# Optimization experiments

Measured on AMD Instinct MI355X. Metric: run time of the kernel, lower is better.

The kernel has to match this reference:

```python
import jax, jax.numpy as jnp
import numpy as np

ALPHA = 0.2          # LeakyReLU negative slope
NEG_INF = -9e15      # mask value from the torch source
N, F_IN, F_OUT = 8192, 128, 64


def setup_inputs() -> dict:
    key = jax.random.key(0)
    k1, k2, k3, k4, k5 = jax.random.split(key, 5)
    X = jax.random.normal(k1, (N, F_IN), dtype=jnp.float32)
    A = jax.random.randint(k2, (N, N), 0, 2, dtype=jnp.int32)  # 0/1 adjacency
    W = jax.random.normal(k3, (F_IN, F_OUT), dtype=jnp.float32) * 0.05
    a1 = jax.random.normal(k4, (F_OUT,), dtype=jnp.float32) * 0.05
    a2 = jax.random.normal(k5, (F_OUT,), dtype=jnp.float32) * 0.05
    return {"X": X, "A": A, "W": W, "a1": a1, "a2": a2}


def reference(X, A, W, a1, a2):
    # h = W(X)  (Linear, no bias)
    h = X @ W                                   # (N, F_out)
    # a([h_i || h_j]) == h_i @ a1 + h_j @ a2  (split of the 2F attention vector)
    s1 = h @ a1                                 # (N,)
    s2 = h @ a2                                 # (N,)
    e = jax.nn.leaky_relu(s1[:, None] + s2[None, :], ALPHA)  # (N, N)
    att = jnp.where(A > 0, e, NEG_INF)
    att = jax.nn.softmax(att, axis=1)           # row-wise masked softmax
    # dropout p=0.0 -> identity
    return att @ h                              # (N, F_out)
```

## Files before the change

### kernel.cpp

```cpp
#include <hip/hip_runtime.h>
#include <hip/hip_bf16.h>

#define NV 8192
#define FIN 128
#define FOUT 64

typedef __attribute__((ext_vector_type(8))) short short8;
typedef __attribute__((ext_vector_type(4))) float floatx4;

__device__ __forceinline__ uint f2bf_u(float f) {
  uint u = __float_as_uint(f);
  return (u + 0x7FFFu + ((u >> 16) & 1u)) >> 16;
}
__device__ __forceinline__ float bf2f(ushort b) {
  return __uint_as_float(((uint)b) << 16);
}

__global__ void k0_detect(const uint* __restrict__ X, int* __restrict__ flag) {
  const int lane = threadIdx.x & 63;
  uint u = X[lane];
  uint e = (u >> 7) & 0xFF;
  bool ok = (e >= 100u) && (e <= 135u);
  unsigned long long b = __ballot(ok);
  if (lane == 0) *flag = (__builtin_popcountll(b) >= 48) ? 1 : 0;
}

__global__ __launch_bounds__(256) void k1_proj(
    const void* __restrict__ Xv, const void* __restrict__ Wv,
    const void* __restrict__ a1v_, const void* __restrict__ a2v_,
    ushort* __restrict__ HtT, float* __restrict__ s1, float* __restrict__ s2,
    const int* __restrict__ flagp)
{
  const int is_bf16 = *flagp;
  const int wave = threadIdx.x >> 6;
  const int lane = threadIdx.x & 63;
  const int i0 = blockIdx.x * 64 + wave * 16;
  const int col = lane & 15;
  const int q   = lane >> 4;

  short8 bfrag[4][4];
  float a1f[4], a2f[4];
  if (is_bf16) {
    const ushort* W = (const ushort*)Wv;
#pragma unroll
    for (int nt = 0; nt < 4; ++nt)
#pragma unroll
      for (int kc = 0; kc < 4; ++kc) {
        short8 b;
#pragma unroll
        for (int j = 0; j < 8; ++j)
          b[j] = (short)W[(kc*32 + q*8 + j)*FOUT + nt*16 + col];
        bfrag[nt][kc] = b;
      }
#pragma unroll
    for (int nt = 0; nt < 4; ++nt) {
      a1f[nt] = bf2f(((const ushort*)a1v_)[nt*16 + col]);
      a2f[nt] = bf2f(((const ushort*)a2v_)[nt*16 + col]);
    }
  } else {
    const float* W = (const float*)Wv;
#pragma unroll
    for (int nt = 0; nt < 4; ++nt)
#pragma unroll
      for (int kc = 0; kc < 4; ++kc) {
        short8 b;
#pragma unroll
        for (int j = 0; j < 8; ++j)
          b[j] = (short)f2bf_u(W[(kc*32 + q*8 + j)*FOUT + nt*16 + col]);
        bfrag[nt][kc] = b;
      }
#pragma unroll
    for (int nt = 0; nt < 4; ++nt) {
      a1f[nt] = ((const float*)a1v_)[nt*16 + col];
      a2f[nt] = ((const float*)a2v_)[nt*16 + col];
    }
  }

  floatx4 acc[4] = {{0.f,0.f,0.f,0.f},{0.f,0.f,0.f,0.f},
                    {0.f,0.f,0.f,0.f},{0.f,0.f,0.f,0.f}};
#pragma unroll
  for (int kc = 0; kc < 4; ++kc) {
    short8 a;
    if (is_bf16) {
      a = *(const short8*)&((const ushort*)Xv)[(size_t)(i0 + col)*FIN + kc*32 + q*8];
    } else {
      const float* X = (const float*)Xv;
      float4 x0 = *(const float4*)&X[(size_t)(i0 + col)*FIN + kc*32 + q*8];
      float4 x1 = *(const float4*)&X[(size_t)(i0 + col)*FIN + kc*32 + q*8 + 4];
      a[0] = (short)f2bf_u(x0.x); a[1] = (short)f2bf_u(x0.y);
      a[2] = (short)f2bf_u(x0.z); a[3] = (short)f2bf_u(x0.w);
      a[4] = (short)f2bf_u(x1.x); a[5] = (short)f2bf_u(x1.y);
      a[6] = (short)f2bf_u(x1.z); a[7] = (short)f2bf_u(x1.w);
    }
#pragma unroll
    for (int nt = 0; nt < 4; ++nt)
      acc[nt] = __builtin_amdgcn_mfma_f32_16x16x32_bf16(a, bfrag[nt][kc], acc[nt], 0, 0, 0);
  }

  float s1p[4] = {0,0,0,0}, s2p[4] = {0,0,0,0};
#pragma unroll
  for (int nt = 0; nt < 4; ++nt) {
    ushort4 pk;
    pk.x = (ushort)f2bf_u(acc[nt][0]);
    pk.y = (ushort)f2bf_u(acc[nt][1]);
    pk.z = (ushort)f2bf_u(acc[nt][2]);
    pk.w = (ushort)f2bf_u(acc[nt][3]);
    *(ushort4*)&HtT[(size_t)(nt*16 + col)*NV + i0 + q*4] = pk;
#pragma unroll
    for (int reg = 0; reg < 4; ++reg) {
      s1p[reg] += acc[nt][reg] * a1f[nt];
      s2p[reg] += acc[nt][reg] * a2f[nt];
    }
  }
#pragma unroll
  for (int m = 1; m < 16; m <<= 1)
#pragma unroll
    for (int reg = 0; reg < 4; ++reg) {
      s1p[reg] += __shfl_xor(s1p[reg], m, 64);
      s2p[reg] += __shfl_xor(s2p[reg], m, 64);
    }
  if (col == 0)
#pragma unroll
    for (int reg = 0; reg < 4; ++reg) {
      s1[i0 + q*4 + reg] = s1p[reg];
      s2[i0 + q*4 + reg] = s2p[reg];
    }
}

#define CT 256
#define NTILES (NV / CT)
#define PSTR (CT + 8)

__global__ __launch_bounds__(256) void k2_attn(
    const int* __restrict__ A, const ushort* __restrict__ HtT,
    const float* __restrict__ s1g, const float* __restrict__ s2g,
    void* __restrict__ outv, const int* __restrict__ flagp)
{
  __shared__ __align__(16) ushort Pl[16 * PSTR];
  __shared__ __align__(16) ushort Hl[64 * PSTR];
  __shared__ float Lrow[16];

  const int is_bf16 = *flagp;
  const int tid   = threadIdx.x;
  const int wave  = tid >> 6;
  const int lane  = tid & 63;
  const int i0    = blockIdx.x * 16;
  const int rbase = wave * 4;
  const int q     = lane >> 4;
  const int mcol  = lane & 15;
  const int srow  = tid >> 5;
  const int scol  = (tid & 31) * 8;

  float s1v[4];
#pragma unroll
  for (int rr = 0; rr < 4; ++rr) s1v[rr] = s1g[i0 + rbase + rr];

  float Lp[4] = {0,0,0,0};
  floatx4 acc = {0.f,0.f,0.f,0.f};

  for (int t = 0; t < NTILES; ++t) {
    const int c0 = t * CT;
    int4 av[4];
#pragma unroll
    for (int rr = 0; rr < 4; ++rr)
      av[rr] = *(const int4*)&A[(size_t)(i0 + rbase + rr)*NV + c0 + lane*4];
    float4 s2v = *(const float4*)&s2g[c0 + lane*4];
    short8 hv[8];
#pragma unroll
    for (int it = 0; it < 8; ++it)
      hv[it] = *(const short8*)&HtT[(size_t)(srow + 8*it)*NV + c0 + scol];

    __syncthreads();

#pragma unroll
    for (int rr = 0; rr < 4; ++rr) {
      const int4 a = av[rr];
      const float s1r = s1v[rr];
      float x0 = s1r + s2v.x, x1 = s1r + s2v.y, x2 = s1r + s2v.z, x3 = s1r + s2v.w;
      float w0 = a.x ? __expf(fmaxf(x0, 0.2f*x0)) : 0.f;
      float w1 = a.y ? __expf(fmaxf(x1, 0.2f*x1)) : 0.f;
      float w2 = a.z ? __expf(fmaxf(x2, 0.2f*x2)) : 0.f;
      float w3 = a.w ? __expf(fmaxf(x3, 0.2f*x3)) : 0.f;
      Lp[rr] += (w0 + w1) + (w2 + w3);
      uint2 pk;
      pk.x = f2bf_u(w0) | (f2bf_u(w1) << 16);
      pk.y = f2bf_u(w2) | (f2bf_u(w3) << 16);
      *(uint2*)&Pl[(rbase + rr)*PSTR + lane*4] = pk;
    }
#pragma unroll
    for (int it = 0; it < 8; ++it)
      *(short8*)&Hl[(srow + 8*it)*PSTR + scol] = hv[it];

    __syncthreads();

#pragma unroll
    for (int kc = 0; kc < 8; ++kc) {
      short8 af = *(const short8*)&Pl[mcol*PSTR + kc*32 + q*8];
      short8 bf = *(const short8*)&Hl[(wave*16 + mcol)*PSTR + kc*32 + q*8];
      acc = __builtin_amdgcn_mfma_f32_16x16x32_bf16(af, bf, acc, 0, 0, 0);
    }
  }

#pragma unroll
  for (int m = 1; m < 64; m <<= 1)
#pragma unroll
    for (int rr = 0; rr < 4; ++rr) Lp[rr] += __shfl_xor(Lp[rr], m, 64);
  if (lane == 0)
#pragma unroll
    for (int rr = 0; rr < 4; ++rr) Lrow[rbase + rr] = Lp[rr];
  __syncthreads();

#pragma unroll
  for (int reg = 0; reg < 4; ++reg) {
    int r = q*4 + reg;
    float v = acc[reg] / Lrow[r];
    if (is_bf16)
      ((ushort*)outv)[(size_t)(i0 + r)*FOUT + wave*16 + mcol] = (ushort)f2bf_u(v);
    else
      ((float*)outv)[(size_t)(i0 + r)*FOUT + wave*16 + mcol] = v;
  }
}

extern "C" void kernel_launch(void* const* d_in, const int* in_sizes, int n_in,
                              void* d_out, int out_size, void* d_ws, size_t ws_size,
                              hipStream_t stream) {
  const void* X  = d_in[0];
  const int*  A  = (const int*)d_in[1];
  const void* W  = d_in[2];
  const void* a1 = d_in[3];
  const void* a2 = d_in[4];

  char* ws = (char*)d_ws;
  ushort* HtT  = (ushort*)ws;
  float*  s1   = (float*)(ws + (size_t)FOUT*NV*2);
  float*  s2   = s1 + NV;
  int*    flag = (int*)(s2 + NV);

  hipLaunchKernelGGL(k0_detect, dim3(1), dim3(64), 0, stream,
                     (const uint*)X, flag);
  hipLaunchKernelGGL(k1_proj, dim3(NV/64), dim3(256), 0, stream,
                     X, W, a1, a2, HtT, s1, s2, flag);
  hipLaunchKernelGGL(k2_attn, dim3(NV/16), dim3(256), 0, stream,
                     A, HtT, s1, s2, d_out, flag);
}
```

Baseline: 383.8 us.

## Split attention column tiles across waves and drop per-tile block barriers

Each wave now takes its own 64-column slice of every 256-column tile and computes all 16 rows by 64 features of partial output. It reads the H fragments straight from global memory instead of staging them in shared memory, and it keeps a private P buffer, so both per-tile __syncthreads are gone. The four per-wave partial accumulators and row sums are combined through shared memory once at the end. The price is more accumulator registers and uncoalesced strided global loads of HtT done by every wave.

```diff
diff --git a/kernel.cpp b/kernel.cpp
--- a/kernel.cpp
+++ b/kernel.cpp
@@ -129,48 +129,51 @@
 
 #define CT 256
 #define NTILES (NV / CT)
-#define PSTR (CT + 8)
+#define PST 72
 
 __global__ __launch_bounds__(256) void k2_attn(
     const int* __restrict__ A, const ushort* __restrict__ HtT,
     const float* __restrict__ s1g, const float* __restrict__ s2g,
     void* __restrict__ outv, const int* __restrict__ flagp)
 {
-  __shared__ __align__(16) ushort Pl[16 * PSTR];
-  __shared__ __align__(16) ushort Hl[64 * PSTR];
-  __shared__ float Lrow[16];
+  __shared__ __align__(16) ushort Pl[4][16 * PST];
+  __shared__ __align__(16) float Red[4][16][64];
+  __shared__ float Lw[4][16];
 
   const int is_bf16 = *flagp;
-  const int tid   = threadIdx.x;
-  const int wave  = tid >> 6;
-  const int lane  = tid & 63;
-  const int i0    = blockIdx.x * 16;
-  const int rbase = wave * 4;
-  const int q     = lane >> 4;
-  const int mcol  = lane & 15;
-  const int srow  = tid >> 5;
-  const int scol  = (tid & 31) * 8;
+  const int tid  = threadIdx.x;
+  const int wave = tid >> 6;
+  const int lane = tid & 63;
+  const int i0   = blockIdx.x * 16;
+  const int q    = lane >> 4;
+  const int mcol = lane & 15;
+
+  ushort* Pw = &Pl[wave][0];
 
   float s1v[4];
 #pragma unroll
-  for (int rr = 0; rr < 4; ++rr) s1v[rr] = s1g[i0 + rbase + rr];
+  for (int rr = 0; rr < 4; ++rr) s1v[rr] = s1g[i0 + q*4 + rr];
+
+  size_t arow[4], hrow[4];
+#pragma unroll
+  for (int rr = 0; rr < 4; ++rr)
+    arow[rr] = (size_t)(i0 + q*4 + rr) * NV + mcol*4;
+#pragma unroll
+  for (int nt = 0; nt < 4; ++nt)
+    hrow[nt] = (size_t)(nt*16 + mcol) * NV + q*8;
 
   float Lp[4] = {0,0,0,0};
-  floatx4 acc = {0.f,0.f,0.f,0.f};
-
+  floatx4 acc[4] = {{0.f,0.f,0.f,0.f},{0.f,0.f,0.f,0.f},
+                    {0.f,0.f,0.f,0.f},{0.f,0.f,0.f,0.f}};
+
+#pragma unroll 2
   for (int t = 0; t < NTILES; ++t) {
-    const int c0 = t * CT;
+    const int c = t*CT + wave*64;
     int4 av[4];
 #pragma unroll
     for (int rr = 0; rr < 4; ++rr)
-      av[rr] = *(const int4*)&A[(size_t)(i0 + rbase + rr)*NV + c0 + lane*4];
-    float4 s2v = *(const float4*)&s2g[c0 + lane*4];
-    short8 hv[8];
-#pragma unroll
-    for (int it = 0; it < 8; ++it)
-      hv[it] = *(const short8*)&HtT[(size_t)(srow + 8*it)*NV + c0 + scol];
-
-    __syncthreads();
+      av[rr] = *(const int4*)&A[arow[rr] + c];
+    float4 s2v = *(const float4*)&s2g[c + mcol*4];
 
 #pragma unroll
     for (int rr = 0; rr < 4; ++rr) {
@@ -185,39 +188,57 @@
       uint2 pk;
       pk.x = f2bf_u(w0) | (f2bf_u(w1) << 16);
       pk.y = f2bf_u(w2) | (f2bf_u(w3) << 16);
-      *(uint2*)&Pl[(rbase + rr)*PSTR + lane*4] = pk;
-    }
-#pragma unroll
-    for (int it = 0; it < 8; ++it)
-      *(short8*)&Hl[(srow + 8*it)*PSTR + scol] = hv[it];
-
-    __syncthreads();
-
-#pragma unroll
-    for (int kc = 0; kc < 8; ++kc) {
-      short8 af = *(const short8*)&Pl[mcol*PSTR + kc*32 + q*8];
-      short8 bf = *(const short8*)&Hl[(wave*16 + mcol)*PSTR + kc*32 + q*8];
-      acc = __builtin_amdgcn_mfma_f32_16x16x32_bf16(af, bf, acc, 0, 0, 0);
-    }
-  }
-
-#pragma unroll
-  for (int m = 1; m < 64; m <<= 1)
+      *(uint2*)&Pw[(q*4 + rr)*PST + mcol*4] = pk;
+    }
+
+#pragma unroll
+    for (int kc2 = 0; kc2 < 2; ++kc2) {
+      short8 af = *(const short8*)&Pw[mcol*PST + kc2*32 + q*8];
+#pragma unroll
+      for (int nt = 0; nt < 4; ++nt) {
+        short8 bf = *(const short8*)&HtT[hrow[nt] + c + kc2*32];
+        acc[nt] = __builtin_amdgcn_mfma_f32_16x16x32_bf16(af, bf, acc[nt], 0, 0, 0);
+      }
+    }
+  }
+
+#pragma unroll
+  for (int m = 1; m < 16; m <<= 1)
 #pragma unroll
     for (int rr = 0; rr < 4; ++rr) Lp[rr] += __shfl_xor(Lp[rr], m, 64);
-  if (lane == 0)
-#pragma unroll
-    for (int rr = 0; rr < 4; ++rr) Lrow[rbase + rr] = Lp[rr];
+  if (mcol == 0)
+#pragma unroll
+    for (int rr = 0; rr < 4; ++rr) Lw[wave][q*4 + rr] = Lp[rr];
+
+#pragma unroll
+  for (int nt = 0; nt < 4; ++nt)
+#pragma unroll
+    for (int reg = 0; reg < 4; ++reg)
+      Red[wave][q*4 + reg][nt*16 + mcol] = acc[nt][reg];
+
   __syncthreads();
 
-#pragma unroll
-  for (int reg = 0; reg < 4; ++reg) {
-    int r = q*4 + reg;
-    float v = acc[reg] / Lrow[r];
-    if (is_bf16)
-      ((ushort*)outv)[(size_t)(i0 + r)*FOUT + wave*16 + mcol] = (ushort)f2bf_u(v);
-    else
-      ((float*)outv)[(size_t)(i0 + r)*FOUT + wave*16 + mcol] = v;
+  {
+    const int r  = tid >> 4;
+    const int fb = (tid & 15) * 4;
+    float4 s = {0.f, 0.f, 0.f, 0.f};
+    float L = 0.f;
+#pragma unroll
+    for (int w = 0; w < 4; ++w) {
+      float4 v = *(const float4*)&Red[w][r][fb];
+      s.x += v.x; s.y += v.y; s.z += v.z; s.w += v.w;
+      L += Lw[w][r];
+    }
+    const float inv = __frcp_rn(L);
+    s.x *= inv; s.y *= inv; s.z *= inv; s.w *= inv;
+    if (is_bf16) {
+      ushort4 pk;
+      pk.x = (ushort)f2bf_u(s.x); pk.y = (ushort)f2bf_u(s.y);
+      pk.z = (ushort)f2bf_u(s.z); pk.w = (ushort)f2bf_u(s.w);
+      *(ushort4*)&((ushort*)outv)[(size_t)(i0 + r)*FOUT + fb] = pk;
+    } else {
+      *(float4*)&((float*)outv)[(size_t)(i0 + r)*FOUT + fb] = s;
+    }
   }
 }
 
```

After: 404.5 us. +5.4%, slower.

## Prefetch next attention tile into registers and shrink column tile to 128

Applied to the files above, without the earlier changes.

The attention kernel now loads the next tile's adjacency, s2 and H values into registers right after the LDS barrier, so those global loads overlap the MFMA work on the current tile. The column tile drops from 256 to 128 and thread mapping changes to one row per 16 threads with 8 columns each, which halves LDS use. Launch bounds now request 6 blocks per multiprocessor. The aim is to hide the latency of streaming the adjacency matrix from memory, at the cost of twice as many loop iterations and barriers.

```diff
diff --git a/kernel.cpp b/kernel.cpp
--- a/kernel.cpp
+++ b/kernel.cpp
@@ -127,97 +127,104 @@
     }
 }
 
-#define CT 256
-#define NTILES (NV / CT)
-#define PSTR (CT + 8)
-
-__global__ __launch_bounds__(256) void k2_attn(
+#define CT 128
+#define NT (NV / CT)
+#define PST 136
+
+__global__ __launch_bounds__(256, 6) void k2_attn(
     const int* __restrict__ A, const ushort* __restrict__ HtT,
     const float* __restrict__ s1g, const float* __restrict__ s2g,
     void* __restrict__ outv, const int* __restrict__ flagp)
 {
-  __shared__ __align__(16) ushort Pl[16 * PSTR];
-  __shared__ __align__(16) ushort Hl[64 * PSTR];
+  __shared__ __align__(16) ushort Pl[16 * PST];
+  __shared__ __align__(16) ushort Hl[64 * PST];
   __shared__ float Lrow[16];
 
   const int is_bf16 = *flagp;
-  const int tid   = threadIdx.x;
-  const int wave  = tid >> 6;
-  const int lane  = tid & 63;
-  const int i0    = blockIdx.x * 16;
-  const int rbase = wave * 4;
-  const int q     = lane >> 4;
-  const int mcol  = lane & 15;
-  const int srow  = tid >> 5;
-  const int scol  = (tid & 31) * 8;
-
-  float s1v[4];
-#pragma unroll
-  for (int rr = 0; rr < 4; ++rr) s1v[rr] = s1g[i0 + rbase + rr];
-
-  float Lp[4] = {0,0,0,0};
-  floatx4 acc = {0.f,0.f,0.f,0.f};
-
-  for (int t = 0; t < NTILES; ++t) {
-    const int c0 = t * CT;
-    int4 av[4];
-#pragma unroll
-    for (int rr = 0; rr < 4; ++rr)
-      av[rr] = *(const int4*)&A[(size_t)(i0 + rbase + rr)*NV + c0 + lane*4];
-    float4 s2v = *(const float4*)&s2g[c0 + lane*4];
-    short8 hv[8];
-#pragma unroll
-    for (int it = 0; it < 8; ++it)
-      hv[it] = *(const short8*)&HtT[(size_t)(srow + 8*it)*NV + c0 + scol];
-
+  const int tid  = threadIdx.x;
+  const int wave = tid >> 6;
+  const int lane = tid & 63;
+  const int i0   = blockIdx.x * 16;
+  const int q    = lane >> 4;
+  const int mcol = lane & 15;
+  const int r    = tid >> 4;
+  const int cb   = (tid & 15) * 8;
+
+  const float s1r = s1g[i0 + r];
+  const size_t abase = (size_t)(i0 + r) * NV + cb;
+
+  float Lp = 0.f;
+  floatx4 acc = {0.f, 0.f, 0.f, 0.f};
+
+  int4 av0 = *(const int4*)&A[abase];
+  int4 av1 = *(const int4*)&A[abase + 4];
+  float4 sv0 = *(const float4*)&s2g[cb];
+  float4 sv1 = *(const float4*)&s2g[cb + 4];
+  short8 hv[4];
+#pragma unroll
+  for (int it = 0; it < 4; ++it)
+    hv[it] = *(const short8*)&HtT[(size_t)(r + 16*it) * NV + cb];
+
+  for (int t = 0; t < NT; ++t) {
     __syncthreads();
 
-#pragma unroll
-    for (int rr = 0; rr < 4; ++rr) {
-      const int4 a = av[rr];
-      const float s1r = s1v[rr];
-      float x0 = s1r + s2v.x, x1 = s1r + s2v.y, x2 = s1r + s2v.z, x3 = s1r + s2v.w;
-      float w0 = a.x ? __expf(fmaxf(x0, 0.2f*x0)) : 0.f;
-      float w1 = a.y ? __expf(fmaxf(x1, 0.2f*x1)) : 0.f;
-      float w2 = a.z ? __expf(fmaxf(x2, 0.2f*x2)) : 0.f;
-      float w3 = a.w ? __expf(fmaxf(x3, 0.2f*x3)) : 0.f;
-      Lp[rr] += (w0 + w1) + (w2 + w3);
-      uint2 pk;
+    {
+      float x0 = s1r + sv0.x, x1 = s1r + sv0.y, x2 = s1r + sv0.z, x3 = s1r + sv0.w;
+      float x4 = s1r + sv1.x, x5 = s1r + sv1.y, x6 = s1r + sv1.z, x7 = s1r + sv1.w;
+      float w0 = av0.x ? __expf(fmaxf(x0, 0.2f*x0)) : 0.f;
+      float w1 = av0.y ? __expf(fmaxf(x1, 0.2f*x1)) : 0.f;
+      float w2 = av0.z ? __expf(fmaxf(x2, 0.2f*x2)) : 0.f;
+      float w3 = av0.w ? __expf(fmaxf(x3, 0.2f*x3)) : 0.f;
+      float w4 = av1.x ? __expf(fmaxf(x4, 0.2f*x4)) : 0.f;
+      float w5 = av1.y ? __expf(fmaxf(x5, 0.2f*x5)) : 0.f;
+      float w6 = av1.z ? __expf(fmaxf(x6, 0.2f*x6)) : 0.f;
+      float w7 = av1.w ? __expf(fmaxf(x7, 0.2f*x7)) : 0.f;
+      Lp += ((w0 + w1) + (w2 + w3)) + ((w4 + w5) + (w6 + w7));
+      uint4 pk;
       pk.x = f2bf_u(w0) | (f2bf_u(w1) << 16);
       pk.y = f2bf_u(w2) | (f2bf_u(w3) << 16);
-      *(uint2*)&Pl[(rbase + rr)*PSTR + lane*4] = pk;
-    }
-#pragma unroll
-    for (int it = 0; it < 8; ++it)
-      *(short8*)&Hl[(srow + 8*it)*PSTR + scol] = hv[it];
+      pk.z = f2bf_u(w4) | (f2bf_u(w5) << 16);
+      pk.w = f2bf_u(w6) | (f2bf_u(w7) << 16);
+      *(uint4*)&Pl[r * PST + cb] = pk;
+#pragma unroll
+      for (int it = 0; it < 4; ++it)
+        *(short8*)&Hl[(r + 16*it) * PST + cb] = hv[it];
+    }
 
     __syncthreads();
 
-#pragma unroll
-    for (int kc = 0; kc < 8; ++kc) {
-      short8 af = *(const short8*)&Pl[mcol*PSTR + kc*32 + q*8];
-      short8 bf = *(const short8*)&Hl[(wave*16 + mcol)*PSTR + kc*32 + q*8];
+    if (t + 1 < NT) {
+      const int c = (t + 1) * CT;
+      av0 = *(const int4*)&A[abase + c];
+      av1 = *(const int4*)&A[abase + c + 4];
+      sv0 = *(const float4*)&s2g[c + cb];
+      sv1 = *(const float4*)&s2g[c + cb + 4];
+#pragma unroll
+      for (int it = 0; it < 4; ++it)
+        hv[it] = *(const short8*)&HtT[(size_t)(r + 16*it) * NV + c + cb];
+    }
+
+#pragma unroll
+    for (int kc = 0; kc < 4; ++kc) {
+      short8 af = *(const short8*)&Pl[mcol * PST + kc*32 + q*8];
+      short8 bf = *(const short8*)&Hl[(wave*16 + mcol) * PST + kc*32 + q*8];
       acc = __builtin_amdgcn_mfma_f32_16x16x32_bf16(af, bf, acc, 0, 0, 0);
     }
   }
 
 #pragma unroll
-  for (int m = 1; m < 64; m <<= 1)
-#pragma unroll
-    for (int rr = 0; rr < 4; ++rr) Lp[rr] += __shfl_xor(Lp[rr], m, 64);
-  if (lane == 0)
-#pragma unroll
-    for (int rr = 0; rr < 4; ++rr) Lrow[rbase + rr] = Lp[rr];
+  for (int m = 1; m < 16; m <<= 1) Lp += __shfl_xor(Lp, m, 64);
+  if (mcol == 0) Lrow[r] = Lp;
   __syncthreads();
 
 #pragma unroll
   for (int reg = 0; reg < 4; ++reg) {
-    int r = q*4 + reg;
-    float v = acc[reg] / Lrow[r];
+    int rr = q*4 + reg;
+    float v = acc[reg] / Lrow[rr];
     if (is_bf16)
-      ((ushort*)outv)[(size_t)(i0 + r)*FOUT + wave*16 + mcol] = (ushort)f2bf_u(v);
+      ((ushort*)outv)[(size_t)(i0 + rr)*FOUT + wave*16 + mcol] = (ushort)f2bf_u(v);
     else
-      ((float*)outv)[(size_t)(i0 + r)*FOUT + wave*16 + mcol] = v;
+      ((float*)outv)[(size_t)(i0 + rr)*FOUT + wave*16 + mcol] = v;
   }
 }
 
```

After: 380.6 us. Within noise of the previous version (-0.8%).
